# Kernel tuning notes

Measured on AMD Instinct MI355X. Metric: run time of the kernel, lower is better.

## Reference

```python
import jax, jax.numpy as jnp
import numpy as np

K = 65536        # codebook_size
D = 32           # code_dim
B, T = 8, 4096
CHUNK = 2048     # search_chunk_size
SIGMA2 = 0.001   # diveq_sigma2
EPS = 1e-8


def setup_inputs() -> dict:
    key = jax.random.key(0)
    k1, k2, k3, k4 = jax.random.split(key, 4)
    z = jax.random.normal(k1, (B, T, D), dtype=jnp.float32)
    codebook = jax.random.normal(k2, (K, D), dtype=jnp.float32) * D ** (-0.5)
    W = jax.random.normal(k3, (D, D), dtype=jnp.float32) * D ** (-0.5)
    proj_bias = jnp.zeros((D,), dtype=jnp.float32)
    noise = jax.random.normal(k4, (B, T, D), dtype=jnp.float32)
    return {"z": z, "codebook": codebook, "W": W, "proj_bias": proj_bias, "noise": noise}


def _chunked_argmin(z_flat, cb):
    """Exact NN search over codebook, scanning CHUNK-sized blocks to bound memory."""
    n_blocks = K // CHUNK  # K divisible by CHUNK here, no padding needed
    blocks = cb.reshape(n_blocks, CHUNK, D)
    offsets = jnp.arange(n_blocks, dtype=jnp.int32) * CHUNK
    z_norm = jnp.sum(z_flat ** 2, axis=1, keepdims=True)  # (N,1)

    def step(carry, xs):
        best_dist, best_idx = carry
        block, off = xs
        emb_norm = jnp.sum(block ** 2, axis=1)                 # (CHUNK,)
        dists = z_norm + emb_norm[None, :] - 2.0 * (z_flat @ block.T)  # (N, CHUNK)
        chunk_arg = jnp.argmin(dists, axis=1).astype(jnp.int32)
        chunk_min = jnp.take_along_axis(dists, chunk_arg[:, None], axis=1)[:, 0]
        better = chunk_min < best_dist
        best_dist = jnp.where(better, chunk_min, best_dist)
        best_idx = jnp.where(better, off + chunk_arg, best_idx)
        return (best_dist, best_idx), None

    N = z_flat.shape[0]
    init = (jnp.full((N,), jnp.inf, dtype=z_flat.dtype),
            jnp.zeros((N,), dtype=jnp.int32))
    (_, best_idx), _ = jax.lax.scan(step, init, (blocks, offsets))
    return best_idx


def reference(z, codebook, W, proj_bias, noise):
    Bz, Tz, C = z.shape
    # projected codebook; raw codebook is stop-gradient'ed as in the original
    cb = jax.lax.stop_gradient(codebook) @ W + proj_bias          # (K, D)
    z_flat = z.reshape(Bz * Tz, C)
    idx = _chunked_argmin(z_flat, cb)                             # (N,) int32
    quant = jnp.take(cb, idx, axis=0).reshape(Bz, Tz, C)

    # noisy quantization (train=True path)
    diff = quant - z
    eps = jnp.asarray(EPS, z.dtype)
    diff_norm = jnp.maximum(jnp.linalg.norm(diff, axis=-1, keepdims=True), eps)
    noise_std = jnp.asarray(SIGMA2 ** 0.5, z.dtype)
    diff_dir = noise_std * noise + diff
    dir_norm = jnp.maximum(jnp.linalg.norm(diff_dir, axis=-1, keepdims=True), eps)
    direction = jax.lax.stop_gradient(diff_dir / dir_norm)
    z_q = z + diff_norm * direction

    # codebook stats
    counts = jnp.zeros((K,), z.dtype).at[idx].add(1.0)
    total = jnp.maximum(jnp.sum(counts), jnp.asarray(1.0, z.dtype))
    avg_probs = counts / total
    safe_probs = jnp.where(avg_probs > 0, avg_probs, jnp.asarray(1.0, z.dtype))
    perplexity = jnp.exp(-jnp.sum(avg_probs * jnp.log(safe_probs + 1e-10)))
    usage_ratio = jnp.mean((counts > 0).astype(z.dtype))

    return z_q, perplexity, usage_ratio, idx.reshape(Bz, Tz)
```

## Files before the change

kernel.cpp:

```cpp
#include <hip/hip_runtime.h>
#include <math.h>

#define KCB 65536
#define DIM 32
#define NQ  32768
#define KSPLIT 8
#define CPS (KCB / KSPLIT)
#define STAGE_C 128
#define NSTAGE (CPS / STAGE_C)
#define QB  256
#define NQB (NQ / QB)
#define ROWB 144
#define ROWS (ROWB/2)
#define NZQ (NQ * DIM)
#define MARGIN 1e-3f

#define OFF_CB      ((size_t)0)
#define OFF_CBN     (OFF_CB + (size_t)KCB * DIM)
#define OFF_PD1     (OFF_CBN + KCB)
#define OFF_PD2     (OFF_PD1 + (size_t)NQ * KSPLIT)
#define OFF_PI1     (OFF_PD2 + (size_t)NQ * KSPLIT)
#define OFF_FIDX    (OFF_PI1 + (size_t)NQ * KSPLIT)
#define OFF_LIST    (OFF_FIDX + NQ)
#define OFF_COUNTS  (OFF_LIST + NQ)
#define OFF_CNT     (OFF_COUNTS + KCB)
#define OFF_STATS   (OFF_CNT + 1)

typedef __attribute__((ext_vector_type(8))) short bf16x8;
typedef __attribute__((ext_vector_type(4))) short s16x4;
typedef __attribute__((ext_vector_type(4))) float f32x4;

__device__ __forceinline__ unsigned short f2bf(float f) {
    unsigned int u = __builtin_bit_cast(unsigned int, f);
    unsigned int r = (u + 0x7FFFu + ((u >> 16) & 1u)) >> 16;
    return (unsigned short)r;
}
__device__ __forceinline__ float bf2f(unsigned short h) {
    unsigned int u = ((unsigned int)h) << 16;
    return __builtin_bit_cast(float, u);
}

__global__ __launch_bounds__(256) void zero_kernel(float* __restrict__ p, int n) {
    int i = blockIdx.x * 256 + threadIdx.x;
    if (i < n) p[i] = 0.0f;
}

__global__ __launch_bounds__(256) void project_kernel(
    const float* __restrict__ codebook, const float* __restrict__ W,
    const float* __restrict__ bias, float* __restrict__ cb, float* __restrict__ cbn)
{
    __shared__ float Ws[DIM * DIM];
    __shared__ float bs[DIM];
    int tid = threadIdx.x;
#pragma unroll
    for (int r = 0; r < 4; ++r) Ws[tid + 256 * r] = W[tid + 256 * r];
    if (tid < DIM) bs[tid] = bias[tid];
    __syncthreads();
    int k = blockIdx.x * 256 + tid;
    float row[DIM];
    const float4* src = (const float4*)(codebook + (size_t)k * DIM);
#pragma unroll
    for (int c = 0; c < 8; ++c) {
        float4 v = src[c];
        row[4*c] = v.x; row[4*c+1] = v.y; row[4*c+2] = v.z; row[4*c+3] = v.w;
    }
    float out[DIM];
    double nrm = 0.0;
#pragma unroll
    for (int d = 0; d < DIM; ++d) {
        double acc = 0.0;
#pragma unroll
        for (int j = 0; j < DIM; ++j) acc += (double)row[j] * (double)Ws[j * DIM + d];
        acc += (double)bs[d];
        float o = (float)acc;
        out[d] = o;
        nrm += (double)o * (double)o;
    }
    float4* dst = (float4*)(cb + (size_t)k * DIM);
#pragma unroll
    for (int c = 0; c < 8; ++c)
        dst[c] = make_float4(out[4*c], out[4*c+1], out[4*c+2], out[4*c+3]);
    cbn[k] = (float)nrm;
}

__global__ __launch_bounds__(256) void search_kernel(
    const float* __restrict__ z, const float* __restrict__ cb,
    const float* __restrict__ cbn,
    float* __restrict__ pd1, float* __restrict__ pd2, int* __restrict__ pi1)
{
    __shared__ __align__(16) unsigned char smem[2*STAGE_C*ROWB + 2*STAGE_C*4];

    const int tid  = threadIdx.x;
    const int lane = tid & 63;
    const int qg   = tid >> 6;
    const int col  = lane & 15;
    const int kh   = lane >> 4;

    const int split = blockIdx.y;
    const int qblk  = blockIdx.x;
    const int cbase = split * CPS;

    bf16x8 ah[4], al[4];
    {
        const int qrow = qblk * QB + qg * 64;
#pragma unroll
        for (int s = 0; s < 4; ++s) {
            const float* zp = z + (size_t)(qrow + s*16 + col) * DIM + kh*8;
            float4 f0 = *(const float4*)zp;
            float4 f1 = *(const float4*)(zp + 4);
            float zf[8] = {f0.x,f0.y,f0.z,f0.w,f1.x,f1.y,f1.z,f1.w};
#pragma unroll
            for (int j = 0; j < 8; ++j) {
                float m2 = -2.0f * zf[j];
                unsigned short h = f2bf(m2);
                unsigned short l = f2bf(m2 - bf2f(h));
                ah[s][j] = (short)h;
                al[s][j] = (short)l;
            }
        }
    }

    float d1s[4][4], d2s[4][4]; int i1s[4][4];
#pragma unroll
    for (int s = 0; s < 4; ++s)
#pragma unroll
        for (int r = 0; r < 4; ++r) { d1s[s][r] = INFINITY; d2s[s][r] = INFINITY; i1s[s][r] = 0; }

    float4 stg[4]; float stgcn = 0.f;

    auto issue = [&](int st) {
#pragma unroll
        for (int i = 0; i < 4; ++i) {
            int cid = tid + 256 * i;
            int r = cid >> 3, c = cid & 7;
            stg[i] = *(const float4*)(cb + (size_t)(cbase + st*STAGE_C + r) * DIM + c*4);
        }
        if (tid < STAGE_C) stgcn = cbn[cbase + st*STAGE_C + tid];
    };
    auto stage_write = [&](int buf) {
#pragma unroll
        for (int i = 0; i < 4; ++i) {
            int cid = tid + 256 * i;
            int rr = cid >> 3, c = cid & 7;
            float v[4] = {stg[i].x, stg[i].y, stg[i].z, stg[i].w};
            s16x4 hv, lv;
#pragma unroll
            for (int j = 0; j < 4; ++j) {
                unsigned short h = f2bf(v[j]);
                unsigned short l = f2bf(v[j] - bf2f(h));
                hv[j] = (short)h; lv[j] = (short)l;
            }
            short* base = (short*)(smem + buf * (STAGE_C * ROWB)) + rr * ROWS + c * 4;
            *(s16x4*)base        = hv;
            *(s16x4*)(base + 32) = lv;
        }
        if (tid < STAGE_C) {
            float* cnlb = (float*)(smem + 2*STAGE_C*ROWB + buf * (STAGE_C * 4));
            cnlb[tid] = stgcn;
        }
    };

    auto compute = [&](int buf, int sbase) {
        const short* csb  = (const short*)(smem + buf * (STAGE_C * ROWB));
        const float* cnlb = (const float*)(smem + 2*STAGE_C*ROWB + buf * (STAGE_C * 4));
#pragma unroll
        for (int t = 0; t < 8; ++t) {
            const short* brow = csb + (t*16 + col) * ROWS + kh*8;
            bf16x8 bh = *(const bf16x8*)brow;
            bf16x8 bl = *(const bf16x8*)(brow + 32);
            float cnv = cnlb[t*16 + col];
            int idxv = sbase + t*16 + col;
            f32x4 cacc = {cnv, cnv, cnv, cnv};
#pragma unroll
            for (int s = 0; s < 4; ++s) {
                f32x4 acc = cacc;
                acc = __builtin_amdgcn_mfma_f32_16x16x32_bf16(ah[s], bh, acc, 0, 0, 0);
                acc = __builtin_amdgcn_mfma_f32_16x16x32_bf16(ah[s], bl, acc, 0, 0, 0);
                acc = __builtin_amdgcn_mfma_f32_16x16x32_bf16(al[s], bh, acc, 0, 0, 0);
#pragma unroll
                for (int r = 0; r < 4; ++r) {
                    float d   = acc[r];
                    float od1 = d1s[s][r];
                    d2s[s][r] = fminf(fmaxf(d, od1), d2s[s][r]);
                    d1s[s][r] = fminf(d, od1);
                    i1s[s][r] = (d < od1) ? idxv : i1s[s][r];
                }
            }
        }
    };

    issue(0);
    stage_write(0);
    __syncthreads();
    int cur = 0;
    for (int s = 0; s < NSTAGE; ++s) {
        if (s + 1 < NSTAGE) issue(s + 1);
        compute(cur, cbase + s * STAGE_C);
        if (s + 1 < NSTAGE) stage_write(cur ^ 1);
        __syncthreads();
        cur ^= 1;
    }

#pragma unroll
    for (int m = 1; m < 16; m <<= 1) {
#pragma unroll
        for (int s = 0; s < 4; ++s)
#pragma unroll
            for (int r = 0; r < 4; ++r) {
                float od1 = __shfl_xor(d1s[s][r], m);
                float od2 = __shfl_xor(d2s[s][r], m);
                int   oi1 = __shfl_xor(i1s[s][r], m);
                float nd2 = fminf(fminf(d2s[s][r], od2), fmaxf(d1s[s][r], od1));
                i1s[s][r] = (od1 < d1s[s][r]) ? oi1 : i1s[s][r];
                d1s[s][r] = fminf(d1s[s][r], od1);
                d2s[s][r] = nd2;
            }
    }

    if (col == 0) {
        const int qb = qblk * QB + qg * 64;
#pragma unroll
        for (int s = 0; s < 4; ++s)
#pragma unroll
            for (int r = 0; r < 4; ++r) {
                int q = qb + s*16 + kh*4 + r;
                size_t o = (size_t)q * KSPLIT + split;
                pd1[o] = d1s[s][r];
                pd2[o] = d2s[s][r];
                pi1[o] = i1s[s][r];
            }
    }
}

__global__ __launch_bounds__(256) void combine_kernel(
    const float* __restrict__ pd1, const float* __restrict__ pd2,
    const int* __restrict__ pi1,
    int* __restrict__ fidx, int* __restrict__ list, int* __restrict__ cnt)
{
    int q = blockIdx.x * 256 + threadIdx.x;
    if (q >= NQ) return;
    float d1 = INFINITY, d2 = INFINITY;
    int i1 = 0;
#pragma unroll
    for (int s = 0; s < KSPLIT; ++s) {
        float da = pd1[(size_t)q * KSPLIT + s];
        float db = pd2[(size_t)q * KSPLIT + s];
        int   ia = pi1[(size_t)q * KSPLIT + s];
        if (da < d1) { d2 = fminf(d1, db); d1 = da; i1 = ia; }
        else         { d2 = fminf(d2, fminf(da, db)); }
    }
    fidx[q] = i1;
    if (d2 - d1 < MARGIN) {
        int p = atomicAdd(cnt, 1);
        list[p] = q;
    }
}

__global__ __launch_bounds__(256) void recheck_kernel(
    const float* __restrict__ z, const float* __restrict__ cb,
    const int* __restrict__ list, const int* __restrict__ cnt,
    int* __restrict__ fidx)
{
    __shared__ double sd[256];
    __shared__ int    si[256];
    int n = *cnt;
    int tid = threadIdx.x;
    for (int li = blockIdx.x; li < n; li += gridDim.x) {
        int q = list[li];
        const float* zq = z + (size_t)q * DIM;
        double zr[DIM];
#pragma unroll
        for (int d = 0; d < DIM; ++d) zr[d] = (double)zq[d];
        double bd = 1e300;
        int bi = 0;
        for (int k = tid; k < KCB; k += 256) {
            const float* c = cb + (size_t)k * DIM;
            double s = 0.0;
#pragma unroll
            for (int d = 0; d < DIM; ++d) {
                double df = zr[d] - (double)c[d];
                s = fma(df, df, s);
            }
            if (s < bd) { bd = s; bi = k; }
        }
        sd[tid] = bd; si[tid] = bi;
        __syncthreads();
        for (int off = 128; off > 0; off >>= 1) {
            if (tid < off) {
                double od = sd[tid + off]; int oi = si[tid + off];
                if (od < sd[tid] || (od == sd[tid] && oi < si[tid])) { sd[tid] = od; si[tid] = oi; }
            }
            __syncthreads();
        }
        if (tid == 0) fidx[q] = si[0];
        __syncthreads();
    }
}

__global__ __launch_bounds__(256) void rows_kernel(
    const float* __restrict__ z, const float* __restrict__ noise,
    const float* __restrict__ cb, const int* __restrict__ fidx,
    float* __restrict__ out, float* __restrict__ counts)
{
    int q = blockIdx.x * 256 + threadIdx.x;
    if (q >= NQ) return;
    int idx = fidx[q];
    const float4* zp  = (const float4*)(z + (size_t)q * DIM);
    const float4* np_ = (const float4*)(noise + (size_t)q * DIM);
    const float4* cp  = (const float4*)(cb + (size_t)idx * DIM);
    float zr[DIM], nr[DIM], cr[DIM];
#pragma unroll
    for (int c = 0; c < 8; ++c) {
        float4 a = zp[c], b = np_[c], d = cp[c];
        zr[4*c]=a.x; zr[4*c+1]=a.y; zr[4*c+2]=a.z; zr[4*c+3]=a.w;
        nr[4*c]=b.x; nr[4*c+1]=b.y; nr[4*c+2]=b.z; nr[4*c+3]=b.w;
        cr[4*c]=d.x; cr[4*c+1]=d.y; cr[4*c+2]=d.z; cr[4*c+3]=d.w;
    }
    const float noise_std = 0.0316227766016838f;
    float ds = 0.f, dn = 0.f;
    float dd[DIM];
#pragma unroll
    for (int d = 0; d < DIM; ++d) {
        float df = cr[d] - zr[d];
        ds = fmaf(df, df, ds);
        float v = fmaf(noise_std, nr[d], df);
        dd[d] = v;
        dn = fmaf(v, v, dn);
    }
    float diff_norm = fmaxf(sqrtf(ds), 1e-8f);
    float dir_norm  = fmaxf(sqrtf(dn), 1e-8f);
    float scale = diff_norm / dir_norm;
    float4* op = (float4*)(out + (size_t)q * DIM);
#pragma unroll
    for (int c = 0; c < 8; ++c) {
        op[c] = make_float4(fmaf(scale, dd[4*c+0], zr[4*c+0]),
                            fmaf(scale, dd[4*c+1], zr[4*c+1]),
                            fmaf(scale, dd[4*c+2], zr[4*c+2]),
                            fmaf(scale, dd[4*c+3], zr[4*c+3]));
    }
    out[NZQ + 2 + q] = (float)idx;
    atomicAdd(&counts[idx], 1.0f);
}

__global__ __launch_bounds__(256) void stats_kernel(
    const float* __restrict__ counts, float* __restrict__ stats)
{
    int i = blockIdx.x * 256 + threadIdx.x;
    float c = counts[i];
    float p = c * (1.0f / 32768.0f);
    float s = (c > 0.f) ? p * logf(p + 1e-10f) : 0.f;
    float u = (c > 0.f) ? 1.f : 0.f;
#pragma unroll
    for (int off = 32; off > 0; off >>= 1) {
        s += __shfl_down(s, off);
        u += __shfl_down(u, off);
    }
    __shared__ float ss[4], su[4];
    int wid = threadIdx.x >> 6, lane = threadIdx.x & 63;
    if (lane == 0) { ss[wid] = s; su[wid] = u; }
    __syncthreads();
    if (threadIdx.x == 0) {
        atomicAdd(&stats[0], ss[0] + ss[1] + ss[2] + ss[3]);
        atomicAdd(&stats[1], su[0] + su[1] + su[2] + su[3]);
    }
}

__global__ void epilogue_kernel(const float* __restrict__ stats, float* __restrict__ out) {
    if (threadIdx.x == 0) {
        out[NZQ]     = expf(-stats[0]);
        out[NZQ + 1] = stats[1] * (1.0f / 65536.0f);
    }
}

extern "C" void kernel_launch(void* const* d_in, const int* in_sizes, int n_in,
                              void* d_out, int out_size, void* d_ws, size_t ws_size,
                              hipStream_t stream)
{
    const float* z        = (const float*)d_in[0];
    const float* codebook = (const float*)d_in[1];
    const float* W        = (const float*)d_in[2];
    const float* bias     = (const float*)d_in[3];
    const float* noise    = (const float*)d_in[4];
    float* out = (float*)d_out;
    float* ws  = (float*)d_ws;

    float* cb     = ws + OFF_CB;
    float* cbn    = ws + OFF_CBN;
    float* pd1    = ws + OFF_PD1;
    float* pd2    = ws + OFF_PD2;
    int*   pi1    = (int*)(ws + OFF_PI1);
    int*   fidx   = (int*)(ws + OFF_FIDX);
    int*   list   = (int*)(ws + OFF_LIST);
    float* counts = ws + OFF_COUNTS;
    int*   cnt    = (int*)(ws + OFF_CNT);
    float* stats  = ws + OFF_STATS;

    zero_kernel<<<(KCB + 3 + 255) / 256, 256, 0, stream>>>(counts, KCB + 3);
    project_kernel<<<KCB / 256, 256, 0, stream>>>(codebook, W, bias, cb, cbn);
    dim3 sg(NQB, KSPLIT);
    search_kernel<<<sg, 256, 0, stream>>>(z, cb, cbn, pd1, pd2, pi1);
    combine_kernel<<<NQ / 256, 256, 0, stream>>>(pd1, pd2, pi1, fidx, list, cnt);
    recheck_kernel<<<512, 256, 0, stream>>>(z, cb, list, cnt, fidx);
    rows_kernel<<<NQ / 256, 256, 0, stream>>>(z, noise, cb, fidx, out, counts);
    stats_kernel<<<KCB / 256, 256, 0, stream>>>(counts, stats);
    epilogue_kernel<<<1, 64, 0, stream>>>(stats, out);
}
```

Measured before the change: 1.067 ms.

## Pre-split codebook into swizzled bf16 hi/lo tiles in projection kernel

```diff
diff --git a/kernel.cpp b/kernel.cpp
--- a/kernel.cpp
+++ b/kernel.cpp
@@ -10,8 +10,7 @@
 #define NSTAGE (CPS / STAGE_C)
 #define QB  256
 #define NQB (NQ / QB)
-#define ROWB 144
-#define ROWS (ROWB/2)
+#define STAGE_BYTES 16384
 #define NZQ (NQ * DIM)
 #define MARGIN 1e-3f
 
@@ -25,9 +24,10 @@
 #define OFF_COUNTS  (OFF_LIST + NQ)
 #define OFF_CNT     (OFF_COUNTS + KCB)
 #define OFF_STATS   (OFF_CNT + 1)
+#define OFF_CBSWZ   (OFF_STATS + 2)
 
 typedef __attribute__((ext_vector_type(8))) short bf16x8;
-typedef __attribute__((ext_vector_type(4))) short s16x4;
+typedef __attribute__((ext_vector_type(8))) short s16x8;
 typedef __attribute__((ext_vector_type(4))) float f32x4;
 
 __device__ __forceinline__ unsigned short f2bf(float f) {
@@ -40,14 +40,10 @@
     return __builtin_bit_cast(float, u);
 }
 
-__global__ __launch_bounds__(256) void zero_kernel(float* __restrict__ p, int n) {
-    int i = blockIdx.x * 256 + threadIdx.x;
-    if (i < n) p[i] = 0.0f;
-}
-
 __global__ __launch_bounds__(256) void project_kernel(
     const float* __restrict__ codebook, const float* __restrict__ W,
-    const float* __restrict__ bias, float* __restrict__ cb, float* __restrict__ cbn)
+    const float* __restrict__ bias, float* __restrict__ cb, float* __restrict__ cbn,
+    float* __restrict__ cbswz, float* __restrict__ counts)
 {
     __shared__ float Ws[DIM * DIM];
     __shared__ float bs[DIM];
@@ -81,14 +77,34 @@
     for (int c = 0; c < 8; ++c)
         dst[c] = make_float4(out[4*c], out[4*c+1], out[4*c+2], out[4*c+3]);
     cbn[k] = (float)nrm;
-}
-
-__global__ __launch_bounds__(256) void search_kernel(
-    const float* __restrict__ z, const float* __restrict__ cb,
+
+    {
+        int tile = k >> 7, t = (k >> 4) & 7, col = k & 15;
+        char* base = (char*)cbswz + (size_t)tile * STAGE_BYTES + t * 2048;
+#pragma unroll
+        for (int kh = 0; kh < 4; ++kh) {
+            s16x8 hv, lv;
+#pragma unroll
+            for (int j = 0; j < 8; ++j) {
+                float v = out[kh*8 + j];
+                unsigned short h = f2bf(v);
+                hv[j] = (short)h;
+                lv[j] = (short)f2bf(v - bf2f(h));
+            }
+            *(s16x8*)(base + (kh*16 + col) * 16)        = hv;
+            *(s16x8*)(base + 1024 + (kh*16 + col) * 16) = lv;
+        }
+    }
+    counts[k] = 0.0f;
+    if (k < 3) counts[KCB + k] = 0.0f;
+}
+
+__global__ __launch_bounds__(256, 3) void search_kernel(
+    const float* __restrict__ z, const float* __restrict__ cbswz,
     const float* __restrict__ cbn,
     float* __restrict__ pd1, float* __restrict__ pd2, int* __restrict__ pi1)
 {
-    __shared__ __align__(16) unsigned char smem[2*STAGE_C*ROWB + 2*STAGE_C*4];
+    __shared__ __align__(16) unsigned char smem[2*STAGE_BYTES + 2*STAGE_C*4];
 
     const int tid  = threadIdx.x;
     const int lane = tid & 63;
@@ -129,45 +145,29 @@
     float4 stg[4]; float stgcn = 0.f;
 
     auto issue = [&](int st) {
-#pragma unroll
-        for (int i = 0; i < 4; ++i) {
-            int cid = tid + 256 * i;
-            int r = cid >> 3, c = cid & 7;
-            stg[i] = *(const float4*)(cb + (size_t)(cbase + st*STAGE_C + r) * DIM + c*4);
-        }
+        const float4* src = (const float4*)((const char*)cbswz
+                          + (size_t)(cbase / STAGE_C + st) * STAGE_BYTES);
+#pragma unroll
+        for (int i = 0; i < 4; ++i) stg[i] = src[tid + 256 * i];
         if (tid < STAGE_C) stgcn = cbn[cbase + st*STAGE_C + tid];
     };
     auto stage_write = [&](int buf) {
-#pragma unroll
-        for (int i = 0; i < 4; ++i) {
-            int cid = tid + 256 * i;
-            int rr = cid >> 3, c = cid & 7;
-            float v[4] = {stg[i].x, stg[i].y, stg[i].z, stg[i].w};
-            s16x4 hv, lv;
-#pragma unroll
-            for (int j = 0; j < 4; ++j) {
-                unsigned short h = f2bf(v[j]);
-                unsigned short l = f2bf(v[j] - bf2f(h));
-                hv[j] = (short)h; lv[j] = (short)l;
-            }
-            short* base = (short*)(smem + buf * (STAGE_C * ROWB)) + rr * ROWS + c * 4;
-            *(s16x4*)base        = hv;
-            *(s16x4*)(base + 32) = lv;
-        }
+        float4* dst = (float4*)(smem + buf * STAGE_BYTES);
+#pragma unroll
+        for (int i = 0; i < 4; ++i) dst[tid + 256 * i] = stg[i];
         if (tid < STAGE_C) {
-            float* cnlb = (float*)(smem + 2*STAGE_C*ROWB + buf * (STAGE_C * 4));
+            float* cnlb = (float*)(smem + 2*STAGE_BYTES + buf * (STAGE_C * 4));
             cnlb[tid] = stgcn;
         }
     };
 
     auto compute = [&](int buf, int sbase) {
-        const short* csb  = (const short*)(smem + buf * (STAGE_C * ROWB));
-        const float* cnlb = (const float*)(smem + 2*STAGE_C*ROWB + buf * (STAGE_C * 4));
+        const char*  csb  = (const char*)smem + buf * STAGE_BYTES;
+        const float* cnlb = (const float*)(smem + 2*STAGE_BYTES + buf * (STAGE_C * 4));
 #pragma unroll
         for (int t = 0; t < 8; ++t) {
-            const short* brow = csb + (t*16 + col) * ROWS + kh*8;
-            bf16x8 bh = *(const bf16x8*)brow;
-            bf16x8 bl = *(const bf16x8*)(brow + 32);
+            bf16x8 bh = *(const bf16x8*)(csb + t*2048 + lane*16);
+            bf16x8 bl = *(const bf16x8*)(csb + t*2048 + 1024 + lane*16);
             float cnv = cnlb[t*16 + col];
             int idxv = sbase + t*16 + col;
             f32x4 cacc = {cnv, cnv, cnv, cnv};
@@ -394,11 +394,11 @@
     float* counts = ws + OFF_COUNTS;
     int*   cnt    = (int*)(ws + OFF_CNT);
     float* stats  = ws + OFF_STATS;
-
-    zero_kernel<<<(KCB + 3 + 255) / 256, 256, 0, stream>>>(counts, KCB + 3);
-    project_kernel<<<KCB / 256, 256, 0, stream>>>(codebook, W, bias, cb, cbn);
+    float* cbswz  = ws + OFF_CBSWZ;
+
+    project_kernel<<<KCB / 256, 256, 0, stream>>>(codebook, W, bias, cb, cbn, cbswz, counts);
     dim3 sg(NQB, KSPLIT);
-    search_kernel<<<sg, 256, 0, stream>>>(z, cb, cbn, pd1, pd2, pi1);
+    search_kernel<<<sg, 256, 0, stream>>>(z, cbswz, cbn, pd1, pd2, pi1);
     combine_kernel<<<NQ / 256, 256, 0, stream>>>(pd1, pd2, pi1, fidx, list, cnt);
     recheck_kernel<<<512, 256, 0, stream>>>(z, cb, list, cnt, fidx);
     rows_kernel<<<NQ / 256, 256, 0, stream>>>(z, noise, cb, fidx, out, counts);
```

Result: slower. 2.121 ms (+98.7%).
